# Kernel optimization log

Hardware: AMD Instinct MI355X
Metric: run time of the kernel (lower is better)

The kernel has to match this reference:

```python
import jax, jax.numpy as jnp
import numpy as np


def log_g(x):
    # log of g(x) = where(x>=0, x+0.5, sigmoid(x))
    return jnp.where(x >= 0, jnp.log(jax.nn.relu(x) + 0.5), -jax.nn.softplus(-x))


def mingru_layer(x, h0, w, b):
    # x: (B,S,In), h0: (B,1,H), w: (2H,In), b: (2H,)
    B, S, _ = x.shape
    gh = jnp.einsum('bsi,oi->bso', x, w) + b          # (B,S,2H)
    H = gh.shape[-1] // 2
    gate, hidden = gh[..., :H], gh[..., H:]
    log_z = -jax.nn.softplus(-gate)                    # log sigmoid(gate)
    log_coeffs = -jax.nn.softplus(gate)                # log(1 - z)
    log_tilde_h = log_g(hidden)
    log_values = jnp.concatenate([jnp.log(h0), log_z + log_tilde_h], axis=1)  # (B,S+1,H)
    a_star = jnp.concatenate(
        [jnp.zeros((B, 1, H), dtype=x.dtype), jnp.cumsum(log_coeffs, axis=1)], axis=1
    )                                                  # (B,S+1,H)
    log_h = a_star + jax.lax.cumlogsumexp(log_values - a_star, axis=1)
    return jnp.exp(log_h)[:, 1:]                       # (B,S,H)


def setup_inputs() -> dict:
    key = jax.random.key(0)
    k = jax.random.split(key, 5)
    B, S, D, H = 8, 4096, 512, 512
    sc = 1.0 / np.sqrt(D)
    return {
        'x': jax.random.normal(k[0], (B, S, D), jnp.float32),
        'w0': jax.random.normal(k[1], (2 * H, D), jnp.float32) * sc,
        'b0': jax.random.normal(k[2], (2 * H,), jnp.float32) * 0.01,
        'w1': jax.random.normal(k[3], (2 * H, H), jnp.float32) * sc,
        'b1': jax.random.normal(k[4], (2 * H,), jnp.float32) * 0.01,
    }


def reference(x, w0, b0, w1, b1):
    B = x.shape[0]
    # init_hidden_state: g(zeros) = 0.5
    next_hidden = []
    inp = x
    for (w, b) in ((w0, b0), (w1, b1)):
        H = w.shape[0] // 2
        h0 = jnp.full((B, 1, H), 0.5, dtype=x.dtype)
        out = mingru_layer(inp, h0, w, b)
        next_hidden.append(out[:, -1:])
        inp = out
    return (out, jnp.stack(next_hidden))  # (B,S,H), (L,B,1,H)
```

## Files before the change

kernel.cpp:

```cpp
#include <hip/hip_runtime.h>
#include <math.h>


typedef unsigned short u16;
typedef __attribute__((ext_vector_type(8))) short short8;
typedef __attribute__((ext_vector_type(4))) float f32x4;

__device__ __forceinline__ u16 f2bf(float f) {
    unsigned int u = __float_as_uint(f);
    return (u16)((u + 0x7fffu + ((u >> 16) & 1u)) >> 16);
}
__device__ __forceinline__ float bf2f(u16 u) {
    return __uint_as_float(((unsigned int)u) << 16);
}
__device__ __forceinline__ void async16(const void* g, void* l) {
    __builtin_amdgcn_global_load_lds(
        (const __attribute__((address_space(1))) unsigned int*)g,
        (__attribute__((address_space(3))) unsigned int*)l, 16, 0, 0);
}
__device__ __forceinline__ float fastrcp(float x) { return __builtin_amdgcn_rcpf(x); }

__device__ __forceinline__ void coeff_val(float gate, float hid, float& c, float& v)
{
    float cc = fastrcp(1.0f + __expf(gate));
    float gp = hid + 0.5f;
    float gn = fastrcp(1.0f + __expf(-hid));
    float g  = (hid >= 0.0f) ? gp : gn;
    c = cc;
    v = (1.0f - cc) * g;
}

__global__ __launch_bounds__(256) void cast3(
    const float* __restrict__ x,  u16* __restrict__ xb,  int nx4,
    const float* __restrict__ w0, u16* __restrict__ w0b,
    const float* __restrict__ w1, u16* __restrict__ w1b, int nw4)
{
    int i = blockIdx.x * 256 + threadIdx.x;
    const float* src; u16* dst; int idx;
    if (i < nx4)                { src = x;  dst = xb;  idx = i; }
    else if (i < nx4 + nw4)     { src = w0; dst = w0b; idx = i - nx4; }
    else if (i < nx4 + 2 * nw4) { src = w1; dst = w1b; idx = i - nx4 - nw4; }
    else return;
    float4 v = ((const float4*)src)[idx];
    ushort4 o = make_ushort4(f2bf(v.x), f2bf(v.y), f2bf(v.z), f2bf(v.w));
    ((ushort4*)dst)[idx] = o;
}

#define TST 144

__global__ __launch_bounds__(256) void gemm_fused(
    const u16* __restrict__ A, const u16* __restrict__ W,
    const float* __restrict__ bias, u16* __restrict__ gh,
    float* __restrict__ cA, float* __restrict__ cV, int K)
{
    __shared__ __align__(16) u16 lds[128 * TST];
    __shared__ float2 csum[2][2][64];

    u16* Asm = lds;
    u16* Wsm = lds + 8192;

    const int tid  = threadIdx.x;
    const int d    = blockIdx.y * 8 + blockIdx.x;
    const int cpx  = (int)(gridDim.x * gridDim.y) >> 3;
    const int t0   = (d & 7) * cpx + (d >> 3);
    const int bn   = t0 & 7;
    const int bm   = t0 >> 3;
    const int lane = tid & 63;
    const int wave = tid >> 6;
    const int wm   = (wave >> 1) * 64;
    const int wn   = (wave & 1) * 64;
    const int w1   = wave & 1;
    const int fm   = lane & 15;
    const int kb   = lane >> 4;

    const u16* Ap[4]; const u16* Wp[4]; char* lA[4]; char* lW[4];
    #pragma unroll
    for (int t = 0; t < 4; ++t) {
        const int gt = tid + 256 * t;
        const int r  = gt >> 3;
        const int q  = (gt & 7) ^ (r & 7);
        Ap[t] = A + (size_t)(bm * 128 + r) * K + q * 8;
        const int wr = bn * 64 + (r & 31) + ((r & 64) >> 1) + ((r & 32) ? 512 : 0);
        Wp[t] = W + (size_t)wr * K + q * 8;
        lA[t] = (char*)Asm + gt * 16;
        lW[t] = (char*)Wsm + gt * 16;
    }

    int offA[4], offB[4];
    #pragma unroll
    for (int i = 0; i < 4; ++i) {
        const int rowA = wm + i * 16 + fm;
        offA[i] = rowA * 128 + ((kb ^ (rowA & 7)) * 16);
        const int rowB = wn + i * 16 + fm;
        offB[i] = rowB * 128 + ((kb ^ (rowB & 7)) * 16);
    }

    f32x4 acc[4][4];
    #pragma unroll
    for (int i = 0; i < 4; ++i)
        #pragma unroll
        for (int j = 0; j < 4; ++j)
            acc[i][j] = (f32x4){0.f, 0.f, 0.f, 0.f};

    const char* AsB = (const char*)Asm;
    const char* WsB = (const char*)Wsm;

    for (int kt = 0; kt < K; kt += 64) {
        #pragma unroll
        for (int t = 0; t < 4; ++t) { async16(Ap[t], lA[t]); async16(Wp[t], lW[t]); }
        __syncthreads();
        #pragma unroll
        for (int ks = 0; ks < 2; ++ks) {
            const int xo = ks << 6;
            short8 a[4], b[4];
            #pragma unroll
            for (int i = 0; i < 4; ++i) a[i] = *(const short8*)(AsB + (offA[i] ^ xo));
            #pragma unroll
            for (int j = 0; j < 4; ++j) b[j] = *(const short8*)(WsB + (offB[j] ^ xo));
            #pragma unroll
            for (int i = 0; i < 4; ++i)
                #pragma unroll
                for (int j = 0; j < 4; ++j)
                    acc[i][j] = __builtin_amdgcn_mfma_f32_16x16x32_bf16(
                        a[i], b[j], acc[i][j], 0, 0, 0);
        }
        __syncthreads();
        #pragma unroll
        for (int t = 0; t < 4; ++t) { Ap[t] += 64; Wp[t] += 64; }
    }

    float bg[2], bh[2];
    #pragma unroll
    for (int jj = 0; jj < 2; ++jj) {
        const int chl = w1 * 32 + jj * 16 + fm;
        bg[jj] = bias[bn * 64 + chl];
        bh[jj] = bias[512 + bn * 64 + chl];
    }
    unsigned int* ldsw = (unsigned int*)lds;
    #pragma unroll
    for (int i = 0; i < 4; ++i)
        #pragma unroll
        for (int jj = 0; jj < 2; ++jj) {
            const int chl = w1 * 32 + jj * 16 + fm;
            const f32x4 g4 = acc[i][jj];
            const f32x4 h4 = acc[i][jj + 2];
            #pragma unroll
            for (int r = 0; r < 4; ++r) {
                const int row = wm + i * 16 + kb * 4 + r;
                float c, v;
                coeff_val(g4[r] + bg[jj], h4[r] + bh[jj], c, v);
                ldsw[row * 72 + chl] = (unsigned int)f2bf(c)
                                     | ((unsigned int)f2bf(v) << 16);
            }
        }
    __syncthreads();

    #pragma unroll
    for (int it = 0; it < 8; ++it) {
        const int row = it * 16 + (tid >> 4);
        const int sc  = (tid & 15) * 8;
        short8 vv = *(const short8*)&lds[row * TST + sc];
        *(short8*)&gh[(size_t)(bm * 128 + row) * 1024 + bn * 128 + sc] = vv;
    }

    const int ch   = tid & 63;
    const int half = (tid >> 6) & 1;
    const int ck   = tid >> 7;
    float Aa = 1.f, Vv = 0.f;
    const int rbase = ck * 64 + half * 32;
    #pragma unroll 4
    for (int s = 0; s < 32; ++s) {
        const unsigned int p = ldsw[(rbase + s) * 72 + ch];
        const float c = bf2f((u16)p);
        const float v = bf2f((u16)(p >> 16));
        Aa *= c;
        Vv = fmaf(c, Vv, v);
    }
    csum[ck][half][ch] = make_float2(Aa, Vv);
    __syncthreads();
    if (half == 0) {
        float2 s0 = csum[ck][0][ch];
        float2 s1 = csum[ck][1][ch];
        float Ac = s1.x * s0.x;
        float Vc = fmaf(s1.x, s0.y, s1.y);
        const int b   = bm >> 5;
        const int ckg = (bm & 31) * 2 + ck;
        const size_t idx = ((size_t)(b * 64 + ckg)) * 512 + bn * 64 + ch;
        cA[idx] = Ac;
        cV[idx] = Vc;
    }
}

__global__ __launch_bounds__(256) void scan_pass2(
    const float* __restrict__ cA, const float* __restrict__ cV,
    float* __restrict__ carry, int Nc)
{
    const int tid = threadIdx.x;
    const int b = blockIdx.x;
    float s0 = 0.5f, s1 = 0.5f;
    #pragma unroll 8
    for (int ck = 0; ck < Nc; ++ck) {
        const size_t idx = (size_t)(b * Nc + ck) * 512 + 2 * tid;
        *(float2*)(carry + idx) = make_float2(s0, s1);
        float2 a = *(const float2*)(cA + idx);
        float2 v = *(const float2*)(cV + idx);
        s0 = fmaf(a.x, s0, v.x);
        s1 = fmaf(a.y, s1, v.y);
    }
}

template <bool OUT_BF16>
__global__ __launch_bounds__(256) void scan_pass3(
    const u16* __restrict__ gh, const float* __restrict__ carry,
    void* __restrict__ outv, float* __restrict__ nh,
    int S, int Lc, int Nc)
{
    const int tid = threadIdx.x;
    const int b  = blockIdx.x / Nc;
    const int ck = blockIdx.x % Nc;
    const u16* base = gh + (size_t)(b * S + ck * Lc) * 1024 + 4 * tid;
    const size_t cidx = (size_t)(b * Nc + ck) * 512 + 2 * tid;
    float2 st = *(const float2*)(carry + cidx);
    float h0 = st.x, h1 = st.y;
    const size_t obase = (size_t)(b * S + ck * Lc) * 512 + 2 * tid;
    #pragma unroll 4
    for (int s = 0; s < Lc; ++s) {
        ushort4 q = *(const ushort4*)(base + (size_t)s * 1024);
        h0 = fmaf(bf2f(q.x), h0, bf2f(q.y));
        h1 = fmaf(bf2f(q.z), h1, bf2f(q.w));
        if (OUT_BF16) {
            ushort2 o = make_ushort2(f2bf(h0), f2bf(h1));
            *(ushort2*)((u16*)outv + obase + (size_t)s * 512) = o;
        } else {
            *(float2*)((float*)outv + obase + (size_t)s * 512) = make_float2(h0, h1);
        }
    }
    if (ck == Nc - 1)
        *(float2*)(nh + (size_t)b * 512 + 2 * tid) = make_float2(h0, h1);
}

extern "C" void kernel_launch(void* const* d_in, const int* in_sizes, int n_in,
                              void* d_out, int out_size, void* d_ws, size_t ws_size,
                              hipStream_t stream)
{
    const float* x  = (const float*)d_in[0];
    const float* w0 = (const float*)d_in[1];
    const float* b0 = (const float*)d_in[2];
    const float* w1 = (const float*)d_in[3];
    const float* b1 = (const float*)d_in[4];
    float* out = (float*)d_out;

    const int B = 8, S = 4096, K = 512;
    const int M = B * S;
    const int Lc = 64, Nc = S / Lc;

    u16* gh  = (u16*)d_ws;
    u16* xb  = gh  + (size_t)M * 1024;
    u16* h0b = xb  + (size_t)M * 512;
    u16* w0b = h0b + (size_t)M * 512;
    u16* w1b = w0b + (size_t)1024 * 512;
    float* cA    = (float*)(w1b + (size_t)1024 * 512);
    float* cV    = cA + (size_t)B * Nc * 512;
    float* carry = cV + (size_t)B * Nc * 512;

    float* nh0 = out + (size_t)M * 512;
    float* nh1 = nh0 + (size_t)B * 512;

    dim3 blk(256);
    dim3 ggrid(8, M / 128);
    dim3 sgrid(B * Nc);

    const int nx4 = M * K / 4;
    const int nw4 = 1024 * K / 4;
    cast3<<<dim3((nx4 + 2 * nw4 + 255) / 256), blk, 0, stream>>>(
        x, xb, nx4, w0, w0b, w1, w1b, nw4);

    gemm_fused<<<ggrid, blk, 0, stream>>>(xb, w0b, b0, gh, cA, cV, K);
    scan_pass2<<<dim3(B), blk, 0, stream>>>(cA, cV, carry, Nc);
    scan_pass3<true><<<sgrid, blk, 0, stream>>>(gh, carry, h0b, nh0, S, Lc, Nc);

    gemm_fused<<<ggrid, blk, 0, stream>>>(h0b, w1b, b1, gh, cA, cV, K);
    scan_pass2<<<dim3(B), blk, 0, stream>>>(cA, cV, carry, Nc);
    scan_pass3<false><<<sgrid, blk, 0, stream>>>(gh, carry, out, nh1, S, Lc, Nc);
}
```

Baseline: 273.9 us.

## Double-buffer GEMM K-loop with 32-wide stages and shrink scan chunks to 32

The GEMM main loop moves from single-buffered 64-wide K tiles to double-buffered 32-wide tiles, so the async global-to-LDS loads for the next stage are issued before computing the current one. The XOR swizzle and LDS row stride are adjusted to the narrower tile. The in-block chunk scan now uses 32-row chunks per wave, which drops the csum shared array and its extra barrier, while the scan passes process twice as many chunks. The layer-1 activation buffer also aliases the now-dead bf16 x buffer to save workspace. The cost is more loop iterations and barriers per K, plus a longer serial carry pass.

New measurement: 288.2 us. 1.05x slower.

```diff
diff --git a/kernel.cpp b/kernel.cpp
--- a/kernel.cpp
+++ b/kernel.cpp
@@ -46,7 +46,7 @@
     ((ushort4*)dst)[idx] = o;
 }
 
-#define TST 144
+#define TST 136
 
 __global__ __launch_bounds__(256) void gemm_fused(
     const u16* __restrict__ A, const u16* __restrict__ W,
@@ -54,10 +54,6 @@
     float* __restrict__ cA, float* __restrict__ cV, int K)
 {
     __shared__ __align__(16) u16 lds[128 * TST];
-    __shared__ float2 csum[2][2][64];
-
-    u16* Asm = lds;
-    u16* Wsm = lds + 8192;
 
     const int tid  = threadIdx.x;
     const int d    = blockIdx.y * 8 + blockIdx.x;
@@ -73,26 +69,22 @@
     const int fm   = lane & 15;
     const int kb   = lane >> 4;
 
-    const u16* Ap[4]; const u16* Wp[4]; char* lA[4]; char* lW[4];
-    #pragma unroll
-    for (int t = 0; t < 4; ++t) {
-        const int gt = tid + 256 * t;
-        const int r  = gt >> 3;
-        const int q  = (gt & 7) ^ (r & 7);
-        Ap[t] = A + (size_t)(bm * 128 + r) * K + q * 8;
-        const int wr = bn * 64 + (r & 31) + ((r & 64) >> 1) + ((r & 32) ? 512 : 0);
-        Wp[t] = W + (size_t)wr * K + q * 8;
-        lA[t] = (char*)Asm + gt * 16;
-        lW[t] = (char*)Wsm + gt * 16;
-    }
+    const int r0 = tid >> 2, q0 = (tid & 3) ^ (r0 & 3);
+    const int r1 = r0 + 64,  q1 = (tid & 3) ^ (r1 & 3);
+    const u16* Ap0 = A + (size_t)(bm * 128 + r0) * 512 + q0 * 8;
+    const u16* Ap1 = A + (size_t)(bm * 128 + r1) * 512 + q1 * 8;
+    const int wr0 = bn * 64 + (r0 & 31) + ((r0 & 32) ? 512 : 0);
+    const int wr1 = bn * 64 + (r1 & 31) + 32 + ((r1 & 32) ? 512 : 0);
+    const u16* Wp0 = W + (size_t)wr0 * 512 + q0 * 8;
+    const u16* Wp1 = W + (size_t)wr1 * 512 + q1 * 8;
 
     int offA[4], offB[4];
     #pragma unroll
     for (int i = 0; i < 4; ++i) {
         const int rowA = wm + i * 16 + fm;
-        offA[i] = rowA * 128 + ((kb ^ (rowA & 7)) * 16);
+        offA[i] = rowA * 64 + ((kb ^ (rowA & 3)) * 16);
         const int rowB = wn + i * 16 + fm;
-        offB[i] = rowB * 128 + ((kb ^ (rowB & 7)) * 16);
+        offB[i] = rowB * 64 + ((kb ^ (rowB & 3)) * 16);
     }
 
     f32x4 acc[4][4];
@@ -102,32 +94,43 @@
         for (int j = 0; j < 4; ++j)
             acc[i][j] = (f32x4){0.f, 0.f, 0.f, 0.f};
 
-    const char* AsB = (const char*)Asm;
-    const char* WsB = (const char*)Wsm;
-
-    for (int kt = 0; kt < K; kt += 64) {
-        #pragma unroll
-        for (int t = 0; t < 4; ++t) { async16(Ap[t], lA[t]); async16(Wp[t], lW[t]); }
+    const char* AsB = (const char*)lds;
+
+#define STAGE(NB) do { \
+    char* dst_ = (char*)lds + (NB); \
+    async16(Ap0, dst_ + tid * 16); \
+    async16(Ap1, dst_ + (tid + 256) * 16); \
+    async16(Wp0, dst_ + 8192 + tid * 16); \
+    async16(Wp1, dst_ + 8192 + (tid + 256) * 16); \
+    Ap0 += 32; Ap1 += 32; Wp0 += 32; Wp1 += 32; } while (0)
+
+#define COMPUTE(CB) do { \
+    const char* src_ = AsB + (CB); \
+    short8 av[4], bw[4]; \
+    _Pragma("unroll") for (int i = 0; i < 4; ++i) \
+        av[i] = *(const short8*)(src_ + offA[i]); \
+    _Pragma("unroll") for (int j = 0; j < 4; ++j) \
+        bw[j] = *(const short8*)(src_ + 8192 + offB[j]); \
+    _Pragma("unroll") for (int i = 0; i < 4; ++i) \
+        _Pragma("unroll") for (int j = 0; j < 4; ++j) \
+            acc[i][j] = __builtin_amdgcn_mfma_f32_16x16x32_bf16( \
+                av[i], bw[j], acc[i][j], 0, 0, 0); \
+} while (0)
+
+    int cb = 0;
+    STAGE(0);
+    __syncthreads();
+    for (int kt = 32; kt < K; kt += 32) {
+        STAGE(cb ^ 16384);
+        COMPUTE(cb);
         __syncthreads();
-        #pragma unroll
-        for (int ks = 0; ks < 2; ++ks) {
-            const int xo = ks << 6;
-            short8 a[4], b[4];
-            #pragma unroll
-            for (int i = 0; i < 4; ++i) a[i] = *(const short8*)(AsB + (offA[i] ^ xo));
-            #pragma unroll
-            for (int j = 0; j < 4; ++j) b[j] = *(const short8*)(WsB + (offB[j] ^ xo));
-            #pragma unroll
-            for (int i = 0; i < 4; ++i)
-                #pragma unroll
-                for (int j = 0; j < 4; ++j)
-                    acc[i][j] = __builtin_amdgcn_mfma_f32_16x16x32_bf16(
-                        a[i], b[j], acc[i][j], 0, 0, 0);
-        }
-        __syncthreads();
-        #pragma unroll
-        for (int t = 0; t < 4; ++t) { Ap[t] += 64; Wp[t] += 64; }
-    }
+        cb ^= 16384;
+    }
+    COMPUTE(cb);
+    __syncthreads();
+
+#undef STAGE
+#undef COMPUTE
 
     float bg[2], bh[2];
     #pragma unroll
@@ -149,7 +152,7 @@
                 const int row = wm + i * 16 + kb * 4 + r;
                 float c, v;
                 coeff_val(g4[r] + bg[jj], h4[r] + bh[jj], c, v);
-                ldsw[row * 72 + chl] = (unsigned int)f2bf(c)
+                ldsw[row * 68 + chl] = (unsigned int)f2bf(c)
                                      | ((unsigned int)f2bf(v) << 16);
             }
         }
@@ -163,32 +166,22 @@
         *(short8*)&gh[(size_t)(bm * 128 + row) * 1024 + bn * 128 + sc] = vv;
     }
 
-    const int ch   = tid & 63;
-    const int half = (tid >> 6) & 1;
-    const int ck   = tid >> 7;
+    const int ch = tid & 63;
+    const int ck = tid >> 6;
     float Aa = 1.f, Vv = 0.f;
-    const int rbase = ck * 64 + half * 32;
     #pragma unroll 4
     for (int s = 0; s < 32; ++s) {
-        const unsigned int p = ldsw[(rbase + s) * 72 + ch];
+        const unsigned int p = ldsw[(ck * 32 + s) * 68 + ch];
         const float c = bf2f((u16)p);
         const float v = bf2f((u16)(p >> 16));
         Aa *= c;
         Vv = fmaf(c, Vv, v);
     }
-    csum[ck][half][ch] = make_float2(Aa, Vv);
-    __syncthreads();
-    if (half == 0) {
-        float2 s0 = csum[ck][0][ch];
-        float2 s1 = csum[ck][1][ch];
-        float Ac = s1.x * s0.x;
-        float Vc = fmaf(s1.x, s0.y, s1.y);
-        const int b   = bm >> 5;
-        const int ckg = (bm & 31) * 2 + ck;
-        const size_t idx = ((size_t)(b * 64 + ckg)) * 512 + bn * 64 + ch;
-        cA[idx] = Ac;
-        cV[idx] = Vc;
-    }
+    const int bb  = bm >> 5;
+    const int ckg = (bm & 31) * 4 + ck;
+    const size_t idx = ((size_t)(bb * 128 + ckg)) * 512 + bn * 64 + ch;
+    cA[idx] = Aa;
+    cV[idx] = Vv;
 }
 
 __global__ __launch_bounds__(256) void scan_pass2(
@@ -252,12 +245,12 @@
 
     const int B = 8, S = 4096, K = 512;
     const int M = B * S;
-    const int Lc = 64, Nc = S / Lc;
+    const int Lc = 32, Nc = S / Lc;
 
     u16* gh  = (u16*)d_ws;
     u16* xb  = gh  + (size_t)M * 1024;
-    u16* h0b = xb  + (size_t)M * 512;
-    u16* w0b = h0b + (size_t)M * 512;
+    u16* h0b = xb;
+    u16* w0b = xb  + (size_t)M * 512;
     u16* w1b = w0b + (size_t)1024 * 512;
     float* cA    = (float*)(w1b + (size_t)1024 * 512);
     float* cV    = cA + (size_t)B * Nc * 512;
```
